# Kernel optimization log

Measured on AMD Instinct MI355X. Metric: run time of the kernel, lower is better.

Reference implementation:

```python
import jax, jax.numpy as jnp
import numpy as np
import math

D_MODEL = 1024
N_HEADS = 16
D_K = D_MODEL // N_HEADS
BS, SQ, SK = 2, 2048, 2048


def setup_inputs() -> dict:
    key = jax.random.key(0)
    ks = jax.random.split(key, 7)
    q = jax.random.normal(ks[0], (BS, SQ, D_MODEL), dtype=jnp.float32)
    k = jax.random.normal(ks[1], (BS, SK, D_MODEL), dtype=jnp.float32)
    v = jax.random.normal(ks[2], (BS, SK, D_MODEL), dtype=jnp.float32)
    # causal mask: True = masked out (matches torch masked_fill semantics)
    mask = jnp.broadcast_to(
        ~jnp.tril(jnp.ones((SQ, SK), dtype=bool)), (BS, SQ, SK))
    scale = 1.0 / math.sqrt(D_MODEL)
    wq = jax.random.normal(ks[3], (D_MODEL, D_MODEL), dtype=jnp.float32) * scale
    wk = jax.random.normal(ks[4], (D_MODEL, D_MODEL), dtype=jnp.float32) * scale
    wv = jax.random.normal(ks[5], (D_MODEL, D_MODEL), dtype=jnp.float32) * scale
    wo = jax.random.normal(ks[6], (D_MODEL, D_MODEL), dtype=jnp.float32) * scale
    return {"q": q, "k": k, "v": v, "mask": mask,
            "wq": wq, "wk": wk, "wv": wv, "wo": wo}


def reference(q, k, v, mask, wq, wk, wv, wo):
    bs, sq, _ = q.shape
    sk = k.shape[1]
    # nn.Linear(bias=False): x @ W.T ; reshape to heads -> [b, h, s, d_k]
    qh = (q @ wq.T).reshape(bs, sq, N_HEADS, D_K).transpose(0, 2, 1, 3)
    kh = (k @ wk.T).reshape(bs, sk, N_HEADS, D_K).transpose(0, 2, 1, 3)
    vh = (v @ wv.T).reshape(bs, sk, N_HEADS, D_K).transpose(0, 2, 1, 3)
    # scaled dot-product attention, full [b,h,sq,sk] scores (as original)
    z = jnp.einsum('bhqd,bhkd->bhqk', qh, kh) / math.sqrt(D_K)
    z = jnp.where(mask[:, None, :, :], jnp.float32(-1e10), z)
    z = jax.nn.softmax(z, axis=-1)
    z = jnp.einsum('bhqk,bhkd->bhqd', z, vh)
    z = z.transpose(0, 2, 1, 3).reshape(bs, sq, D_MODEL)
    return z @ wo.T
```

## Files before the change

### kernel.cpp

```cpp
#include <hip/hip_runtime.h>
#include <hip/hip_bf16.h>
#include <stdint.h>

typedef short s16x8 __attribute__((ext_vector_type(8)));
typedef float f32x4 __attribute__((ext_vector_type(4)));

#define BSZ 2
#define SQL 2048
#define DMODEL 1024
#define NHEAD 16
#define DKH 64

#if __has_builtin(__builtin_amdgcn_exp2f)
#define EXP2(x) __builtin_amdgcn_exp2f(x)
#else
#define EXP2(x) exp2f(x)
#endif

__device__ __forceinline__ ushort f2bf(float f) {
  uint32_t u = __float_as_uint(f);
  u += 0x7fffu + ((u >> 16) & 1u);
  return (ushort)(u >> 16);
}

__device__ __forceinline__ uint32_t cvtpk_bf16(float lo, float hi) {
  uint32_t r;
  asm("v_cvt_pk_bf16_f32 %0, %1, %2" : "=v"(r) : "v"(lo), "v"(hi));
  return r;
}

__device__ __forceinline__ float rowmax16(float x) {
  x = fmaxf(x, __int_as_float(__builtin_amdgcn_update_dpp(0, __float_as_int(x), 0x121, 0xf, 0xf, true)));
  x = fmaxf(x, __int_as_float(__builtin_amdgcn_update_dpp(0, __float_as_int(x), 0x122, 0xf, 0xf, true)));
  x = fmaxf(x, __int_as_float(__builtin_amdgcn_update_dpp(0, __float_as_int(x), 0x124, 0xf, 0xf, true)));
  x = fmaxf(x, __int_as_float(__builtin_amdgcn_update_dpp(0, __float_as_int(x), 0x128, 0xf, 0xf, true)));
  return x;
}

__device__ __forceinline__ void gload_lds16(const ushort* g, ushort* l) {
  __builtin_amdgcn_global_load_lds((const __attribute__((address_space(1))) void*)g,
                                   (__attribute__((address_space(3))) void*)l,
                                   16, 0, 0);
}

__global__ void cvt_all(const float* __restrict__ q, const float* __restrict__ k,
                        const float* __restrict__ v, const float* __restrict__ wq,
                        const float* __restrict__ wk, const float* __restrict__ wv,
                        const float* __restrict__ wo, ushort* __restrict__ dq,
                        ushort* __restrict__ dk, ushort* __restrict__ dv,
                        ushort* __restrict__ dwq, ushort* __restrict__ dwk,
                        ushort* __restrict__ dwv, ushort* __restrict__ dwo) {
  int b = blockIdx.x;
  const float* s; ushort* d; int off;
  if (b < 4096)       { s = q;  d = dq;  off = b; }
  else if (b < 8192)  { s = k;  d = dk;  off = b - 4096; }
  else if (b < 12288) { s = v;  d = dv;  off = b - 8192; }
  else if (b < 13312) { s = wq; d = dwq; off = b - 12288; }
  else if (b < 14336) { s = wk; d = dwk; off = b - 13312; }
  else if (b < 15360) { s = wv; d = dwv; off = b - 14336; }
  else                { s = wo; d = dwo; off = b - 15360; }
  int i = (off * 256 + threadIdx.x) * 4;
  float4 x = *(const float4*)(s + i);
  ushort4 o;
  o.x = f2bf(x.x); o.y = f2bf(x.y); o.z = f2bf(x.z); o.w = f2bf(x.w);
  *(ushort4*)(d + i) = o;
}

__device__ __forceinline__ void gemm_core(const ushort* __restrict__ A,
                                          const ushort* __restrict__ B,
                                          ushort* sA, ushort* sB, f32x4 (&acc)[4][4]) {
  const int t = threadIdx.x, w = t >> 6, lane = t & 63;
  const int lrow = lane & 15, lk = (lane >> 4) * 8;
  const int m0 = blockIdx.x * 128, n0 = blockIdx.y * 128;
  const int wm = (w >> 1) * 64, wn = (w & 1) * 64;

  auto stage = [&](int kt, int buf) {
#pragma unroll
    for (int i = 0; i < 2; ++i) {
      int ci = i * 256 + t;
      int row = ci >> 2;
      int ce = (ci & 3) * 8;
      gload_lds16(A + (size_t)(m0 + row) * 1024 + kt * 32 + ce,
                  sA + buf * 4096 + (i * 256 + w * 64) * 8);
      gload_lds16(B + (size_t)(n0 + row) * 1024 + kt * 32 + ce,
                  sB + buf * 4096 + (i * 256 + w * 64) * 8);
    }
  };

  stage(0, 0);
  for (int kt = 0; kt < 32; ++kt) {
    const int cur = kt & 1;
    if (kt < 31) {
      stage(kt + 1, cur ^ 1);
      asm volatile("s_waitcnt vmcnt(4)" ::: "memory");
    } else {
      asm volatile("s_waitcnt vmcnt(0)" ::: "memory");
    }
    __builtin_amdgcn_s_barrier();
    __builtin_amdgcn_sched_barrier(0);
    const ushort* pA = sA + cur * 4096;
    const ushort* pB = sB + cur * 4096;
    s16x8 af[4], bfr[4];
#pragma unroll
    for (int mi = 0; mi < 4; ++mi)
      af[mi] = *(const s16x8*)(pA + (wm + mi * 16 + lrow) * 32 + lk);
#pragma unroll
    for (int ni = 0; ni < 4; ++ni)
      bfr[ni] = *(const s16x8*)(pB + (wn + ni * 16 + lrow) * 32 + lk);
    __builtin_amdgcn_s_setprio(1);
#pragma unroll
    for (int mi = 0; mi < 4; ++mi)
#pragma unroll
      for (int ni = 0; ni < 4; ++ni)
        acc[mi][ni] = __builtin_amdgcn_mfma_f32_16x16x32_bf16(af[mi], bfr[ni], acc[mi][ni], 0, 0, 0);
    __builtin_amdgcn_s_setprio(0);
    asm volatile("s_waitcnt lgkmcnt(0)" ::: "memory");
    __builtin_amdgcn_s_barrier();
  }
}

__device__ __forceinline__ void epi_heads(f32x4 (&acc)[4][4], ushort* D, float scale, bool vtrans) {
  const int lane = threadIdx.x & 63, w = threadIdx.x >> 6;
  const int m0 = blockIdx.x * 128, n0 = blockIdx.y * 128;
  const int wm = (w >> 1) * 64, wn = (w & 1) * 64;
#pragma unroll
  for (int mi = 0; mi < 4; ++mi)
#pragma unroll
    for (int ni = 0; ni < 4; ++ni)
#pragma unroll
      for (int r = 0; r < 4; ++r) {
        int m = m0 + wm + mi * 16 + (lane >> 4) * 4 + r;
        int n = n0 + wn + ni * 16 + (lane & 15);
        ushort bv = f2bf(acc[mi][ni][r] * scale);
        int b = m >> 11, s = m & 2047, h = n >> 6, d = n & 63;
        if (vtrans)
          D[((size_t)((b * 16 + h) * 64 + d)) * 2048 + s] = bv;
        else
          D[((size_t)((b * 16 + h) * 2048 + s)) * 64 + d] = bv;
      }
}

__global__ __launch_bounds__(256) void gemm_qkv(const ushort* __restrict__ qb,
                                                const ushort* __restrict__ kb,
                                                const ushort* __restrict__ vb,
                                                const ushort* __restrict__ wqb,
                                                const ushort* __restrict__ wkb,
                                                const ushort* __restrict__ wvb,
                                                ushort* __restrict__ Qh,
                                                ushort* __restrict__ Kh,
                                                ushort* __restrict__ Vt) {
  __shared__ __align__(16) ushort sA[2 * 128 * 32];
  __shared__ __align__(16) ushort sB[2 * 128 * 32];
  const int z = blockIdx.z;
  const ushort* A = (z == 0) ? qb : (z == 1) ? kb : vb;
  const ushort* B = (z == 0) ? wqb : (z == 1) ? wkb : wvb;
  f32x4 acc[4][4] = {};
  gemm_core(A, B, sA, sB, acc);
  ushort* D = (z == 0) ? Qh : (z == 1) ? Kh : Vt;
  epi_heads(acc, D, (z == 0) ? 0.18033688f : 1.0f, z == 2);
}

__global__ __launch_bounds__(256) void gemm_out(const ushort* __restrict__ A,
                                                const ushort* __restrict__ B,
                                                float* __restrict__ D) {
  __shared__ __align__(16) ushort sA[2 * 128 * 32];
  __shared__ __align__(16) ushort sB[2 * 128 * 32];
  f32x4 acc[4][4] = {};
  gemm_core(A, B, sA, sB, acc);
  const int lane = threadIdx.x & 63, w = threadIdx.x >> 6;
  const int m0 = blockIdx.x * 128, n0 = blockIdx.y * 128;
  const int wm = (w >> 1) * 64, wn = (w & 1) * 64;
#pragma unroll
  for (int mi = 0; mi < 4; ++mi)
#pragma unroll
    for (int ni = 0; ni < 4; ++ni)
#pragma unroll
      for (int r = 0; r < 4; ++r) {
        int m = m0 + wm + mi * 16 + (lane >> 4) * 4 + r;
        int n = n0 + wn + ni * 16 + (lane & 15);
        D[(size_t)m * 1024 + n] = acc[mi][ni][r];
      }
}

__global__ __launch_bounds__(512) void attn_fwd(const ushort* __restrict__ Qh,
                                                const ushort* __restrict__ Kh,
                                                const ushort* __restrict__ Vt,
                                                ushort* __restrict__ Z) {
  __shared__ __align__(16) ushort sK[2][64 * 64];
  __shared__ __align__(16) ushort sV[2][64 * 64];
  __shared__ __align__(16) ushort sP[8][16 * 72];
  const int t = threadIdx.x, w = t >> 6, lane = t & 63;
  const int lcol = lane & 15, lhi = lane >> 4;
  const int p = blockIdx.x, bh = blockIdx.y;
  const int qlo = p, qhi = 31 - p;
  const int setid = w >> 2;
  const int qtile = setid ? qhi : qlo;
  const int qr0 = qtile * 64 + (w & 3) * 16;
  const ushort* Qb = Qh + (size_t)bh * SQL * DKH;
  const ushort* Kb = Kh + (size_t)bh * SQL * DKH;
  const ushort* Vb = Vt + (size_t)bh * DKH * SQL;

  s16x8 qf0, qf1;
  {
    const ushort* qp = Qb + (size_t)(qr0 + lcol) * DKH + lhi * 8;
    qf0 = *(const s16x8*)qp;
    qf1 = *(const s16x8*)(qp + 32);
  }
  float mr[4], lrp[4];
  f32x4 o[4] = {};
#pragma unroll
  for (int r = 0; r < 4; ++r) { mr[r] = -1e30f; lrp[r] = 0.f; }
  ushort* Pw = &sP[w][0];

  auto stage = [&](int kb, int buf) {
    int row = t >> 3, cc = t & 7;
    int scz = cc ^ (row & 7);
    gload_lds16(Kb + (size_t)(kb * 64 + row) * DKH + scz * 8, &sK[buf][w * 512]);
    gload_lds16(Vb + (size_t)row * SQL + kb * 64 + scz * 8, &sV[buf][w * 512]);
  };

  const int nkb = qhi + 1;
  stage(0, 0);
  for (int kb = 0; kb < nkb; ++kb) {
    const int cur = kb & 1;
    if (kb + 1 < nkb) {
      stage(kb + 1, cur ^ 1);
      asm volatile("s_waitcnt vmcnt(2)" ::: "memory");
    } else {
      asm volatile("s_waitcnt vmcnt(0)" ::: "memory");
    }
    __builtin_amdgcn_s_barrier();
    __builtin_amdgcn_sched_barrier(0);
    const bool act = setid || (kb <= qlo);
    if (act) {
      const ushort* pK = &sK[cur][0];
      const ushort* pV = &sV[cur][0];
      f32x4 sc4[4];
      __builtin_amdgcn_s_setprio(1);
#pragma unroll
      for (int ktt = 0; ktt < 4; ++ktt) {
        int row = ktt * 16 + lcol;
        int c0 = lhi ^ (row & 7);
        int c1 = (lhi + 4) ^ (row & 7);
        s16x8 k0 = *(const s16x8*)(pK + row * 64 + c0 * 8);
        s16x8 k1 = *(const s16x8*)(pK + row * 64 + c1 * 8);
        f32x4 a = {};
        a = __builtin_amdgcn_mfma_f32_16x16x32_bf16(qf0, k0, a, 0, 0, 0);
        a = __builtin_amdgcn_mfma_f32_16x16x32_bf16(qf1, k1, a, 0, 0, 0);
        sc4[ktt] = a;
      }
      __builtin_amdgcn_s_setprio(0);
      if (kb == qtile) {
#pragma unroll
        for (int ktt = 0; ktt < 4; ++ktt) {
          int kloc = ktt * 16 + lcol;
#pragma unroll
          for (int r = 0; r < 4; ++r)
            if (kloc > (w & 3) * 16 + lhi * 4 + r) sc4[ktt][r] = -1e30f;
        }
      }
      float tm4[4];
#pragma unroll
      for (int r = 0; r < 4; ++r) {
        float tm = fmaxf(fmaxf(sc4[0][r], sc4[1][r]), fmaxf(sc4[2][r], sc4[3][r]));
        tm4[r] = rowmax16(tm);
      }
      bool grow = (tm4[0] > mr[0] + 8.f) || (tm4[1] > mr[1] + 8.f) ||
                  (tm4[2] > mr[2] + 8.f) || (tm4[3] > mr[3] + 8.f);
      if (__any((int)grow)) {
#pragma unroll
        for (int r = 0; r < 4; ++r) {
          float mn = fmaxf(mr[r], tm4[r]);
          float al = EXP2(mr[r] - mn);
          lrp[r] *= al;
          o[0][r] *= al; o[1][r] *= al; o[2][r] *= al; o[3][r] *= al;
          mr[r] = mn;
        }
      }
#pragma unroll
      for (int r = 0; r < 4; ++r) {
        float p0 = EXP2(sc4[0][r] - mr[r]);
        float p1 = EXP2(sc4[1][r] - mr[r]);
        float p2 = EXP2(sc4[2][r] - mr[r]);
        float p3 = EXP2(sc4[3][r] - mr[r]);
        lrp[r] += (p0 + p1) + (p2 + p3);
        uint32_t w01 = cvtpk_bf16(p0, p1);
        uint32_t w23 = cvtpk_bf16(p2, p3);
        ushort* pr = Pw + (lhi * 4 + r) * 72 + lcol;
        pr[0]  = (ushort)(w01 & 0xffffu);
        pr[16] = (ushort)(w01 >> 16);
        pr[32] = (ushort)(w23 & 0xffffu);
        pr[48] = (ushort)(w23 >> 16);
      }
      __builtin_amdgcn_s_setprio(1);
#pragma unroll
      for (int kc = 0; kc < 2; ++kc) {
        s16x8 pf = *(const s16x8*)(Pw + lcol * 72 + kc * 32 + lhi * 8);
#pragma unroll
        for (int dt = 0; dt < 4; ++dt) {
          int row = dt * 16 + lcol;
          int cc = (lhi + 4 * kc) ^ (row & 7);
          s16x8 vf = *(const s16x8*)(pV + row * 64 + cc * 8);
          o[dt] = __builtin_amdgcn_mfma_f32_16x16x32_bf16(pf, vf, o[dt], 0, 0, 0);
        }
      }
      __builtin_amdgcn_s_setprio(0);
    }
    asm volatile("s_waitcnt lgkmcnt(0)" ::: "memory");
    __builtin_amdgcn_s_barrier();
  }

  const int b = bh >> 4, h = bh & 15;
#pragma unroll
  for (int r = 0; r < 4; ++r) {
    float sum = lrp[r];
    sum += __shfl_xor(sum, 1);
    sum += __shfl_xor(sum, 2);
    sum += __shfl_xor(sum, 4);
    sum += __shfl_xor(sum, 8);
    float inv = 1.0f / sum;
    int q = qr0 + lhi * 4 + r;
    size_t base = ((size_t)(b * SQL + q)) * DMODEL + h * DKH + lcol;
#pragma unroll
    for (int dt = 0; dt < 4; ++dt)
      Z[base + dt * 16] = f2bf(o[dt][r] * inv);
  }
}

extern "C" void kernel_launch(void* const* d_in, const int* in_sizes, int n_in,
                              void* d_out, int out_size, void* d_ws, size_t ws_size,
                              hipStream_t stream) {
  const float* q = (const float*)d_in[0];
  const float* k = (const float*)d_in[1];
  const float* v = (const float*)d_in[2];
  const float* wq = (const float*)d_in[4];
  const float* wk = (const float*)d_in[5];
  const float* wv = (const float*)d_in[6];
  const float* wo = (const float*)d_in[7];

  const size_t NBIG = (size_t)BSZ * SQL * DMODEL;
  const size_t NW = (size_t)DMODEL * DMODEL;
  ushort* qb = (ushort*)d_ws;
  ushort* kb = qb + NBIG;
  ushort* vb = kb + NBIG;
  ushort* wqb = vb + NBIG;
  ushort* wkb = wqb + NW;
  ushort* wvb = wkb + NW;
  ushort* wob = wvb + NW;
  ushort* Qh = wob + NW;
  ushort* Kh = Qh + NBIG;
  ushort* Vt = Kh + NBIG;
  ushort* Z  = Vt + NBIG;

  cvt_all<<<dim3(16384), 256, 0, stream>>>(q, k, v, wq, wk, wv, wo,
                                           qb, kb, vb, wqb, wkb, wvb, wob);
  gemm_qkv<<<dim3(32, 8, 3), 256, 0, stream>>>(qb, kb, vb, wqb, wkb, wvb, Qh, Kh, Vt);
  attn_fwd<<<dim3(16, BSZ * NHEAD), 512, 0, stream>>>(Qh, Kh, Vt, Z);
  gemm_out<<<dim3(32, 8), 256, 0, stream>>>(Z, wob, (float*)d_out);
}
```

Measured before the change: 132.0 us.

## Give each attention wave two query subtiles and shrink output GEMM tile

```diff
diff --git a/kernel.cpp b/kernel.cpp
--- a/kernel.cpp
+++ b/kernel.cpp
@@ -133,10 +133,12 @@
         int n = n0 + wn + ni * 16 + (lane & 15);
         ushort bv = f2bf(acc[mi][ni][r] * scale);
         int b = m >> 11, s = m & 2047, h = n >> 6, d = n & 63;
-        if (vtrans)
-          D[((size_t)((b * 16 + h) * 64 + d)) * 2048 + s] = bv;
-        else
+        if (vtrans) {
+          int sp = (s & ~63) | (((s & 15) << 2) | ((s >> 4) & 3));
+          D[((size_t)((b * 16 + h) * 64 + d)) * 2048 + sp] = bv;
+        } else {
           D[((size_t)((b * 16 + h) * 2048 + s)) * 64 + d] = bv;
+        }
       }
 }
 
@@ -160,18 +162,65 @@
   epi_heads(acc, D, (z == 0) ? 0.18033688f : 1.0f, z == 2);
 }
 
-__global__ __launch_bounds__(256) void gemm_out(const ushort* __restrict__ A,
-                                                const ushort* __restrict__ B,
-                                                float* __restrict__ D) {
-  __shared__ __align__(16) ushort sA[2 * 128 * 32];
+__global__ __launch_bounds__(256) void gemm_out64(const ushort* __restrict__ A,
+                                                  const ushort* __restrict__ B,
+                                                  float* __restrict__ D) {
+  __shared__ __align__(16) ushort sA[2 * 64 * 32];
   __shared__ __align__(16) ushort sB[2 * 128 * 32];
-  f32x4 acc[4][4] = {};
-  gemm_core(A, B, sA, sB, acc);
-  const int lane = threadIdx.x & 63, w = threadIdx.x >> 6;
-  const int m0 = blockIdx.x * 128, n0 = blockIdx.y * 128;
-  const int wm = (w >> 1) * 64, wn = (w & 1) * 64;
-#pragma unroll
-  for (int mi = 0; mi < 4; ++mi)
+  const int t = threadIdx.x, w = t >> 6, lane = t & 63;
+  const int lrow = lane & 15, lk = (lane >> 4) * 8;
+  const int m0 = blockIdx.x * 64, n0 = blockIdx.y * 128;
+  const int wm = (w >> 1) * 32, wn = (w & 1) * 64;
+  f32x4 acc[2][4] = {};
+
+  auto stage = [&](int kt, int buf) {
+    {
+      int row = t >> 2, ce = (t & 3) * 8;
+      gload_lds16(A + (size_t)(m0 + row) * 1024 + kt * 32 + ce,
+                  sA + buf * 2048 + (w * 64) * 8);
+    }
+#pragma unroll
+    for (int i = 0; i < 2; ++i) {
+      int ci = i * 256 + t;
+      int row = ci >> 2, ce = (ci & 3) * 8;
+      gload_lds16(B + (size_t)(n0 + row) * 1024 + kt * 32 + ce,
+                  sB + buf * 4096 + (i * 256 + w * 64) * 8);
+    }
+  };
+
+  stage(0, 0);
+  for (int kt = 0; kt < 32; ++kt) {
+    const int cur = kt & 1;
+    if (kt < 31) {
+      stage(kt + 1, cur ^ 1);
+      asm volatile("s_waitcnt vmcnt(3)" ::: "memory");
+    } else {
+      asm volatile("s_waitcnt vmcnt(0)" ::: "memory");
+    }
+    __builtin_amdgcn_s_barrier();
+    __builtin_amdgcn_sched_barrier(0);
+    const ushort* pA = sA + cur * 2048;
+    const ushort* pB = sB + cur * 4096;
+    s16x8 af[2], bfr[4];
+#pragma unroll
+    for (int mi = 0; mi < 2; ++mi)
+      af[mi] = *(const s16x8*)(pA + (wm + mi * 16 + lrow) * 32 + lk);
+#pragma unroll
+    for (int ni = 0; ni < 4; ++ni)
+      bfr[ni] = *(const s16x8*)(pB + (wn + ni * 16 + lrow) * 32 + lk);
+    __builtin_amdgcn_s_setprio(1);
+#pragma unroll
+    for (int mi = 0; mi < 2; ++mi)
+#pragma unroll
+      for (int ni = 0; ni < 4; ++ni)
+        acc[mi][ni] = __builtin_amdgcn_mfma_f32_16x16x32_bf16(af[mi], bfr[ni], acc[mi][ni], 0, 0, 0);
+    __builtin_amdgcn_s_setprio(0);
+    asm volatile("s_waitcnt lgkmcnt(0)" ::: "memory");
+    __builtin_amdgcn_s_barrier();
+  }
+
+#pragma unroll
+  for (int mi = 0; mi < 2; ++mi)
 #pragma unroll
     for (int ni = 0; ni < 4; ++ni)
 #pragma unroll
@@ -182,41 +231,48 @@
       }
 }
 
-__global__ __launch_bounds__(512) void attn_fwd(const ushort* __restrict__ Qh,
+__global__ __launch_bounds__(256) void attn_fwd(const ushort* __restrict__ Qh,
                                                 const ushort* __restrict__ Kh,
                                                 const ushort* __restrict__ Vt,
                                                 ushort* __restrict__ Z) {
   __shared__ __align__(16) ushort sK[2][64 * 64];
   __shared__ __align__(16) ushort sV[2][64 * 64];
-  __shared__ __align__(16) ushort sP[8][16 * 72];
+  __shared__ __align__(16) ushort sP[4][32 * 72];
   const int t = threadIdx.x, w = t >> 6, lane = t & 63;
   const int lcol = lane & 15, lhi = lane >> 4;
   const int p = blockIdx.x, bh = blockIdx.y;
   const int qlo = p, qhi = 31 - p;
-  const int setid = w >> 2;
+  const int setid = w >> 1;
   const int qtile = setid ? qhi : qlo;
-  const int qr0 = qtile * 64 + (w & 3) * 16;
+  const int qr0 = qtile * 64 + (w & 1) * 32;
   const ushort* Qb = Qh + (size_t)bh * SQL * DKH;
   const ushort* Kb = Kh + (size_t)bh * SQL * DKH;
   const ushort* Vb = Vt + (size_t)bh * DKH * SQL;
 
-  s16x8 qf0, qf1;
-  {
-    const ushort* qp = Qb + (size_t)(qr0 + lcol) * DKH + lhi * 8;
-    qf0 = *(const s16x8*)qp;
-    qf1 = *(const s16x8*)(qp + 32);
+  s16x8 qf[2][2];
+#pragma unroll
+  for (int s = 0; s < 2; ++s) {
+    const ushort* qp = Qb + (size_t)(qr0 + s * 16 + lcol) * DKH + lhi * 8;
+    qf[s][0] = *(const s16x8*)qp;
+    qf[s][1] = *(const s16x8*)(qp + 32);
   }
-  float mr[4], lrp[4];
-  f32x4 o[4] = {};
-#pragma unroll
-  for (int r = 0; r < 4; ++r) { mr[r] = -1e30f; lrp[r] = 0.f; }
+  float mr[2][4], lrp[2][4];
+  f32x4 o[2][4] = {};
+#pragma unroll
+  for (int s = 0; s < 2; ++s)
+#pragma unroll
+    for (int r = 0; r < 4; ++r) { mr[s][r] = -1e30f; lrp[s][r] = 0.f; }
   ushort* Pw = &sP[w][0];
 
   auto stage = [&](int kb, int buf) {
-    int row = t >> 3, cc = t & 7;
-    int scz = cc ^ (row & 7);
-    gload_lds16(Kb + (size_t)(kb * 64 + row) * DKH + scz * 8, &sK[buf][w * 512]);
-    gload_lds16(Vb + (size_t)row * SQL + kb * 64 + scz * 8, &sV[buf][w * 512]);
+#pragma unroll
+    for (int i = 0; i < 2; ++i) {
+      int ci = i * 256 + t;
+      int row = ci >> 3, cc = ci & 7;
+      int scz = cc ^ (row & 7);
+      gload_lds16(Kb + (size_t)(kb * 64 + row) * DKH + scz * 8, &sK[buf][(i * 256 + w * 64) * 8]);
+      gload_lds16(Vb + (size_t)row * SQL + kb * 64 + scz * 8, &sV[buf][(i * 256 + w * 64) * 8]);
+    }
   };
 
   const int nkb = qhi + 1;
@@ -225,7 +281,7 @@
     const int cur = kb & 1;
     if (kb + 1 < nkb) {
       stage(kb + 1, cur ^ 1);
-      asm volatile("s_waitcnt vmcnt(2)" ::: "memory");
+      asm volatile("s_waitcnt vmcnt(4)" ::: "memory");
     } else {
       asm volatile("s_waitcnt vmcnt(0)" ::: "memory");
     }
@@ -235,7 +291,7 @@
     if (act) {
       const ushort* pK = &sK[cur][0];
       const ushort* pV = &sV[cur][0];
-      f32x4 sc4[4];
+      f32x4 scs[2][4];
       __builtin_amdgcn_s_setprio(1);
 #pragma unroll
       for (int ktt = 0; ktt < 4; ++ktt) {
@@ -245,63 +301,72 @@
         s16x8 k0 = *(const s16x8*)(pK + row * 64 + c0 * 8);
         s16x8 k1 = *(const s16x8*)(pK + row * 64 + c1 * 8);
         f32x4 a = {};
-        a = __builtin_amdgcn_mfma_f32_16x16x32_bf16(qf0, k0, a, 0, 0, 0);
-        a = __builtin_amdgcn_mfma_f32_16x16x32_bf16(qf1, k1, a, 0, 0, 0);
-        sc4[ktt] = a;
+        a = __builtin_amdgcn_mfma_f32_16x16x32_bf16(qf[0][0], k0, a, 0, 0, 0);
+        a = __builtin_amdgcn_mfma_f32_16x16x32_bf16(qf[0][1], k1, a, 0, 0, 0);
+        scs[0][ktt] = a;
+        f32x4 b2 = {};
+        b2 = __builtin_amdgcn_mfma_f32_16x16x32_bf16(qf[1][0], k0, b2, 0, 0, 0);
+        b2 = __builtin_amdgcn_mfma_f32_16x16x32_bf16(qf[1][1], k1, b2, 0, 0, 0);
+        scs[1][ktt] = b2;
       }
       __builtin_amdgcn_s_setprio(0);
       if (kb == qtile) {
 #pragma unroll
-        for (int ktt = 0; ktt < 4; ++ktt) {
-          int kloc = ktt * 16 + lcol;
-#pragma unroll
-          for (int r = 0; r < 4; ++r)
-            if (kloc > (w & 3) * 16 + lhi * 4 + r) sc4[ktt][r] = -1e30f;
+        for (int s = 0; s < 2; ++s)
+#pragma unroll
+          for (int ktt = 0; ktt < 4; ++ktt) {
+            int kloc = ktt * 16 + lcol;
+#pragma unroll
+            for (int r = 0; r < 4; ++r)
+              if (kloc > (w & 1) * 32 + s * 16 + lhi * 4 + r) scs[s][ktt][r] = -1e30f;
+          }
+      }
+#pragma unroll
+      for (int s = 0; s < 2; ++s) {
+        float tm4[4];
+#pragma unroll
+        for (int r = 0; r < 4; ++r) {
+          float tm = fmaxf(fmaxf(scs[s][0][r], scs[s][1][r]), fmaxf(scs[s][2][r], scs[s][3][r]));
+          tm4[r] = rowmax16(tm);
         }
-      }
-      float tm4[4];
-#pragma unroll
-      for (int r = 0; r < 4; ++r) {
-        float tm = fmaxf(fmaxf(sc4[0][r], sc4[1][r]), fmaxf(sc4[2][r], sc4[3][r]));
-        tm4[r] = rowmax16(tm);
-      }
-      bool grow = (tm4[0] > mr[0] + 8.f) || (tm4[1] > mr[1] + 8.f) ||
-                  (tm4[2] > mr[2] + 8.f) || (tm4[3] > mr[3] + 8.f);
-      if (__any((int)grow)) {
+        bool grow = (tm4[0] > mr[s][0] + 8.f) || (tm4[1] > mr[s][1] + 8.f) ||
+                    (tm4[2] > mr[s][2] + 8.f) || (tm4[3] > mr[s][3] + 8.f);
+        if (__any((int)grow)) {
+#pragma unroll
+          for (int r = 0; r < 4; ++r) {
+            float mn = fmaxf(mr[s][r], tm4[r]);
+            float al = EXP2(mr[s][r] - mn);
+            lrp[s][r] *= al;
+            o[s][0][r] *= al; o[s][1][r] *= al; o[s][2][r] *= al; o[s][3][r] *= al;
+            mr[s][r] = mn;
+          }
+        }
+        ushort* Pws = Pw + s * 16 * 72;
 #pragma unroll
         for (int r = 0; r < 4; ++r) {
-          float mn = fmaxf(mr[r], tm4[r]);
-          float al = EXP2(mr[r] - mn);
-          lrp[r] *= al;
-          o[0][r] *= al; o[1][r] *= al; o[2][r] *= al; o[3][r] *= al;
-          mr[r] = mn;
+          float p0 = EXP2(scs[s][0][r] - mr[s][r]);
+          float p1 = EXP2(scs[s][1][r] - mr[s][r]);
+          float p2 = EXP2(scs[s][2][r] - mr[s][r]);
+          float p3 = EXP2(scs[s][3][r] - mr[s][r]);
+          lrp[s][r] += (p0 + p1) + (p2 + p3);
+          uint2 pk;
+          pk.x = cvtpk_bf16(p0, p1);
+          pk.y = cvtpk_bf16(p2, p3);
+          *(uint2*)(Pws + (lhi * 4 + r) * 72 + lcol * 4) = pk;
         }
       }
-#pragma unroll
-      for (int r = 0; r < 4; ++r) {
-        float p0 = EXP2(sc4[0][r] - mr[r]);
-        float p1 = EXP2(sc4[1][r] - mr[r]);
-        float p2 = EXP2(sc4[2][r] - mr[r]);
-        float p3 = EXP2(sc4[3][r] - mr[r]);
-        lrp[r] += (p0 + p1) + (p2 + p3);
-        uint32_t w01 = cvtpk_bf16(p0, p1);
-        uint32_t w23 = cvtpk_bf16(p2, p3);
-        ushort* pr = Pw + (lhi * 4 + r) * 72 + lcol;
-        pr[0]  = (ushort)(w01 & 0xffffu);
-        pr[16] = (ushort)(w01 >> 16);
-        pr[32] = (ushort)(w23 & 0xffffu);
-        pr[48] = (ushort)(w23 >> 16);
-      }
       __builtin_amdgcn_s_setprio(1);
 #pragma unroll
       for (int kc = 0; kc < 2; ++kc) {
-        s16x8 pf = *(const s16x8*)(Pw + lcol * 72 + kc * 32 + lhi * 8);
+        s16x8 pfA = *(const s16x8*)(Pw + lcol * 72 + kc * 32 + lhi * 8);
+        s16x8 pfB = *(const s16x8*)(Pw + (16 + lcol) * 72 + kc * 32 + lhi * 8);
 #pragma unroll
         for (int dt = 0; dt < 4; ++dt) {
           int row = dt * 16 + lcol;
           int cc = (lhi + 4 * kc) ^ (row & 7);
           s16x8 vf = *(const s16x8*)(pV + row * 64 + cc * 8);
-          o[dt] = __builtin_amdgcn_mfma_f32_16x16x32_bf16(pf, vf, o[dt], 0, 0, 0);
+          o[0][dt] = __builtin_amdgcn_mfma_f32_16x16x32_bf16(pfA, vf, o[0][dt], 0, 0, 0);
+          o[1][dt] = __builtin_amdgcn_mfma_f32_16x16x32_bf16(pfB, vf, o[1][dt], 0, 0, 0);
         }
       }
       __builtin_amdgcn_s_setprio(0);
@@ -312,18 +377,21 @@
 
   const int b = bh >> 4, h = bh & 15;
 #pragma unroll
-  for (int r = 0; r < 4; ++r) {
-    float sum = lrp[r];
-    sum += __shfl_xor(sum, 1);
-    sum += __shfl_xor(sum, 2);
-    sum += __shfl_xor(sum, 4);
-    sum += __shfl_xor(sum, 8);
-    float inv = 1.0f / sum;
-    int q = qr0 + lhi * 4 + r;
-    size_t base = ((size_t)(b * SQL + q)) * DMODEL + h * DKH + lcol;
-#pragma unroll
-    for (int dt = 0; dt < 4; ++dt)
-      Z[base + dt * 16] = f2bf(o[dt][r] * inv);
+  for (int s = 0; s < 2; ++s) {
+#pragma unroll
+    for (int r = 0; r < 4; ++r) {
+      float sum = lrp[s][r];
+      sum += __shfl_xor(sum, 1);
+      sum += __shfl_xor(sum, 2);
+      sum += __shfl_xor(sum, 4);
+      sum += __shfl_xor(sum, 8);
+      float inv = 1.0f / sum;
+      int q = qr0 + s * 16 + lhi * 4 + r;
+      size_t base = ((size_t)(b * SQL + q)) * DMODEL + h * DKH + lcol;
+#pragma unroll
+      for (int dt = 0; dt < 4; ++dt)
+        Z[base + dt * 16] = f2bf(o[s][dt][r] * inv);
+    }
   }
 }
 
@@ -355,6 +423,6 @@
   cvt_all<<<dim3(16384), 256, 0, stream>>>(q, k, v, wq, wk, wv, wo,
                                            qb, kb, vb, wqb, wkb, wvb, wob);
   gemm_qkv<<<dim3(32, 8, 3), 256, 0, stream>>>(qb, kb, vb, wqb, wkb, wvb, Qh, Kh, Vt);
-  attn_fwd<<<dim3(16, BSZ * NHEAD), 512, 0, stream>>>(Qh, Kh, Vt, Z);
-  gemm_out<<<dim3(32, 8), 256, 0, stream>>>(Z, wob, (float*)d_out);
-}
+  attn_fwd<<<dim3(16, BSZ * NHEAD), 256, 0, stream>>>(Qh, Kh, Vt, Z);
+  gemm_out64<<<dim3(64, 8), 256, 0, stream>>>(Z, wob, (float*)d_out);
+}
```

After: 153.8 us. 16.5% more time.

## Fuse activation fp32-to-bf16 conversion into QKV GEMM and shrink output GEMM tiles

Applied to the files above, without the earlier changes.

```diff
diff --git a/kernel.cpp b/kernel.cpp
--- a/kernel.cpp
+++ b/kernel.cpp
@@ -43,80 +43,17 @@
                                    16, 0, 0);
 }
 
-__global__ void cvt_all(const float* __restrict__ q, const float* __restrict__ k,
-                        const float* __restrict__ v, const float* __restrict__ wq,
-                        const float* __restrict__ wk, const float* __restrict__ wv,
-                        const float* __restrict__ wo, ushort* __restrict__ dq,
-                        ushort* __restrict__ dk, ushort* __restrict__ dv,
-                        ushort* __restrict__ dwq, ushort* __restrict__ dwk,
-                        ushort* __restrict__ dwv, ushort* __restrict__ dwo) {
-  int b = blockIdx.x;
-  const float* s; ushort* d; int off;
-  if (b < 4096)       { s = q;  d = dq;  off = b; }
-  else if (b < 8192)  { s = k;  d = dk;  off = b - 4096; }
-  else if (b < 12288) { s = v;  d = dv;  off = b - 8192; }
-  else if (b < 13312) { s = wq; d = dwq; off = b - 12288; }
-  else if (b < 14336) { s = wk; d = dwk; off = b - 13312; }
-  else if (b < 15360) { s = wv; d = dwv; off = b - 14336; }
-  else                { s = wo; d = dwo; off = b - 15360; }
-  int i = (off * 256 + threadIdx.x) * 4;
+__global__ void cvt_w(const float* __restrict__ wq, const float* __restrict__ wk,
+                      const float* __restrict__ wv, const float* __restrict__ wo,
+                      ushort* __restrict__ dwq, ushort* __restrict__ dwk,
+                      ushort* __restrict__ dwv, ushort* __restrict__ dwo) {
+  const float* s = (blockIdx.y == 0) ? wq : (blockIdx.y == 1) ? wk : (blockIdx.y == 2) ? wv : wo;
+  ushort* d = (blockIdx.y == 0) ? dwq : (blockIdx.y == 1) ? dwk : (blockIdx.y == 2) ? dwv : dwo;
+  int i = (blockIdx.x * 256 + threadIdx.x) * 4;
   float4 x = *(const float4*)(s + i);
   ushort4 o;
   o.x = f2bf(x.x); o.y = f2bf(x.y); o.z = f2bf(x.z); o.w = f2bf(x.w);
   *(ushort4*)(d + i) = o;
-}
-
-__device__ __forceinline__ void gemm_core(const ushort* __restrict__ A,
-                                          const ushort* __restrict__ B,
-                                          ushort* sA, ushort* sB, f32x4 (&acc)[4][4]) {
-  const int t = threadIdx.x, w = t >> 6, lane = t & 63;
-  const int lrow = lane & 15, lk = (lane >> 4) * 8;
-  const int m0 = blockIdx.x * 128, n0 = blockIdx.y * 128;
-  const int wm = (w >> 1) * 64, wn = (w & 1) * 64;
-
-  auto stage = [&](int kt, int buf) {
-#pragma unroll
-    for (int i = 0; i < 2; ++i) {
-      int ci = i * 256 + t;
-      int row = ci >> 2;
-      int ce = (ci & 3) * 8;
-      gload_lds16(A + (size_t)(m0 + row) * 1024 + kt * 32 + ce,
-                  sA + buf * 4096 + (i * 256 + w * 64) * 8);
-      gload_lds16(B + (size_t)(n0 + row) * 1024 + kt * 32 + ce,
-                  sB + buf * 4096 + (i * 256 + w * 64) * 8);
-    }
-  };
-
-  stage(0, 0);
-  for (int kt = 0; kt < 32; ++kt) {
-    const int cur = kt & 1;
-    if (kt < 31) {
-      stage(kt + 1, cur ^ 1);
-      asm volatile("s_waitcnt vmcnt(4)" ::: "memory");
-    } else {
-      asm volatile("s_waitcnt vmcnt(0)" ::: "memory");
-    }
-    __builtin_amdgcn_s_barrier();
-    __builtin_amdgcn_sched_barrier(0);
-    const ushort* pA = sA + cur * 4096;
-    const ushort* pB = sB + cur * 4096;
-    s16x8 af[4], bfr[4];
-#pragma unroll
-    for (int mi = 0; mi < 4; ++mi)
-      af[mi] = *(const s16x8*)(pA + (wm + mi * 16 + lrow) * 32 + lk);
-#pragma unroll
-    for (int ni = 0; ni < 4; ++ni)
-      bfr[ni] = *(const s16x8*)(pB + (wn + ni * 16 + lrow) * 32 + lk);
-    __builtin_amdgcn_s_setprio(1);
-#pragma unroll
-    for (int mi = 0; mi < 4; ++mi)
-#pragma unroll
-      for (int ni = 0; ni < 4; ++ni)
-        acc[mi][ni] = __builtin_amdgcn_mfma_f32_16x16x32_bf16(af[mi], bfr[ni], acc[mi][ni], 0, 0, 0);
-    __builtin_amdgcn_s_setprio(0);
-    asm volatile("s_waitcnt lgkmcnt(0)" ::: "memory");
-    __builtin_amdgcn_s_barrier();
-  }
 }
 
 __device__ __forceinline__ void epi_heads(f32x4 (&acc)[4][4], ushort* D, float scale, bool vtrans) {
@@ -133,45 +70,166 @@
         int n = n0 + wn + ni * 16 + (lane & 15);
         ushort bv = f2bf(acc[mi][ni][r] * scale);
         int b = m >> 11, s = m & 2047, h = n >> 6, d = n & 63;
-        if (vtrans)
-          D[((size_t)((b * 16 + h) * 64 + d)) * 2048 + s] = bv;
-        else
+        if (vtrans) {
+          int sp = (s & ~63) | (((s & 15) << 2) | ((s >> 4) & 3));
+          D[((size_t)((b * 16 + h) * 64 + d)) * 2048 + sp] = bv;
+        } else {
           D[((size_t)((b * 16 + h) * 2048 + s)) * 64 + d] = bv;
-      }
-}
-
-__global__ __launch_bounds__(256) void gemm_qkv(const ushort* __restrict__ qb,
-                                                const ushort* __restrict__ kb,
-                                                const ushort* __restrict__ vb,
+        }
+      }
+}
+
+__global__ __launch_bounds__(256) void gemm_qkv(const float* __restrict__ qf,
+                                                const float* __restrict__ kf,
+                                                const float* __restrict__ vf,
                                                 const ushort* __restrict__ wqb,
                                                 const ushort* __restrict__ wkb,
                                                 const ushort* __restrict__ wvb,
                                                 ushort* __restrict__ Qh,
                                                 ushort* __restrict__ Kh,
                                                 ushort* __restrict__ Vt) {
-  __shared__ __align__(16) ushort sA[2 * 128 * 32];
-  __shared__ __align__(16) ushort sB[2 * 128 * 32];
+  __shared__ __align__(16) ushort sA[2 * 4096];
+  __shared__ __align__(16) ushort sB[2 * 4096];
   const int z = blockIdx.z;
-  const ushort* A = (z == 0) ? qb : (z == 1) ? kb : vb;
+  const float* A = (z == 0) ? qf : (z == 1) ? kf : vf;
   const ushort* B = (z == 0) ? wqb : (z == 1) ? wkb : wvb;
+  const int t = threadIdx.x, w = t >> 6, lane = t & 63;
+  const int lrow = lane & 15, lk = (lane >> 4) * 8;
+  const int m0 = blockIdx.x * 128, n0 = blockIdx.y * 128;
+  const int wm = (w >> 1) * 64, wn = (w & 1) * 64;
   f32x4 acc[4][4] = {};
-  gemm_core(A, B, sA, sB, acc);
+
+  const int rowa = t >> 2, cea = (t & 3) * 8;
+  const float* A0 = A + (size_t)(m0 + rowa) * 1024 + cea;
+  const float* A1 = A0 + (size_t)64 * 1024;
+  const int la0 = t * 8, la1 = (256 + t) * 8;
+
+  float4 a00, a01, a10, a11;
+  auto issueA = [&](int kt) {
+    a00 = *(const float4*)(A0 + kt * 32);
+    a01 = *(const float4*)(A0 + kt * 32 + 4);
+    a10 = *(const float4*)(A1 + kt * 32);
+    a11 = *(const float4*)(A1 + kt * 32 + 4);
+  };
+  auto writeA = [&](int buf) {
+    uint4 u0, u1;
+    u0.x = cvtpk_bf16(a00.x, a00.y); u0.y = cvtpk_bf16(a00.z, a00.w);
+    u0.z = cvtpk_bf16(a01.x, a01.y); u0.w = cvtpk_bf16(a01.z, a01.w);
+    u1.x = cvtpk_bf16(a10.x, a10.y); u1.y = cvtpk_bf16(a10.z, a10.w);
+    u1.z = cvtpk_bf16(a11.x, a11.y); u1.w = cvtpk_bf16(a11.z, a11.w);
+    *(uint4*)(sA + buf * 4096 + la0) = u0;
+    *(uint4*)(sA + buf * 4096 + la1) = u1;
+  };
+  auto gloadB = [&](int kt, int buf) {
+#pragma unroll
+    for (int i = 0; i < 2; ++i) {
+      int ci = i * 256 + t, row = ci >> 2, ce = (ci & 3) * 8;
+      gload_lds16(B + (size_t)(n0 + row) * 1024 + kt * 32 + ce,
+                  sB + buf * 4096 + (i * 256 + w * 64) * 8);
+    }
+  };
+
+  issueA(0);
+  gloadB(0, 0);
+  writeA(0);
+  asm volatile("s_waitcnt lgkmcnt(0)" ::: "memory");
+
+  for (int kt = 0; kt < 32; ++kt) {
+    const int cur = kt & 1;
+    if (kt < 31) {
+      issueA(kt + 1);
+      __builtin_amdgcn_sched_barrier(0);
+      gloadB(kt + 1, cur ^ 1);
+      asm volatile("s_waitcnt vmcnt(6)" ::: "memory");
+    } else {
+      asm volatile("s_waitcnt vmcnt(0)" ::: "memory");
+    }
+    __builtin_amdgcn_s_barrier();
+    __builtin_amdgcn_sched_barrier(0);
+    const ushort* pA = sA + cur * 4096;
+    const ushort* pB = sB + cur * 4096;
+    s16x8 af[4], bfr[4];
+#pragma unroll
+    for (int mi = 0; mi < 4; ++mi)
+      af[mi] = *(const s16x8*)(pA + (wm + mi * 16 + lrow) * 32 + lk);
+#pragma unroll
+    for (int ni = 0; ni < 4; ++ni)
+      bfr[ni] = *(const s16x8*)(pB + (wn + ni * 16 + lrow) * 32 + lk);
+    __builtin_amdgcn_s_setprio(1);
+#pragma unroll
+    for (int mi = 0; mi < 4; ++mi)
+#pragma unroll
+      for (int ni = 0; ni < 4; ++ni)
+        acc[mi][ni] = __builtin_amdgcn_mfma_f32_16x16x32_bf16(af[mi], bfr[ni], acc[mi][ni], 0, 0, 0);
+    __builtin_amdgcn_s_setprio(0);
+    if (kt < 31) writeA(cur ^ 1);
+    asm volatile("s_waitcnt lgkmcnt(0)" ::: "memory");
+    __builtin_amdgcn_s_barrier();
+  }
+
   ushort* D = (z == 0) ? Qh : (z == 1) ? Kh : Vt;
   epi_heads(acc, D, (z == 0) ? 0.18033688f : 1.0f, z == 2);
 }
 
-__global__ __launch_bounds__(256) void gemm_out(const ushort* __restrict__ A,
-                                                const ushort* __restrict__ B,
-                                                float* __restrict__ D) {
-  __shared__ __align__(16) ushort sA[2 * 128 * 32];
+__global__ __launch_bounds__(256) void gemm_out64(const ushort* __restrict__ A,
+                                                  const ushort* __restrict__ B,
+                                                  float* __restrict__ D) {
+  __shared__ __align__(16) ushort sA[2 * 64 * 32];
   __shared__ __align__(16) ushort sB[2 * 128 * 32];
-  f32x4 acc[4][4] = {};
-  gemm_core(A, B, sA, sB, acc);
-  const int lane = threadIdx.x & 63, w = threadIdx.x >> 6;
-  const int m0 = blockIdx.x * 128, n0 = blockIdx.y * 128;
-  const int wm = (w >> 1) * 64, wn = (w & 1) * 64;
-#pragma unroll
-  for (int mi = 0; mi < 4; ++mi)
+  const int t = threadIdx.x, w = t >> 6, lane = t & 63;
+  const int lrow = lane & 15, lk = (lane >> 4) * 8;
+  const int m0 = blockIdx.x * 64, n0 = blockIdx.y * 128;
+  const int wm = (w >> 1) * 32, wn = (w & 1) * 64;
+  f32x4 acc[2][4] = {};
+
+  auto stage = [&](int kt, int buf) {
+    {
+      int row = t >> 2, ce = (t & 3) * 8;
+      gload_lds16(A + (size_t)(m0 + row) * 1024 + kt * 32 + ce,
+                  sA + buf * 2048 + (w * 64) * 8);
+    }
+#pragma unroll
+    for (int i = 0; i < 2; ++i) {
+      int ci = i * 256 + t;
+      int row = ci >> 2, ce = (ci & 3) * 8;
+      gload_lds16(B + (size_t)(n0 + row) * 1024 + kt * 32 + ce,
+                  sB + buf * 4096 + (i * 256 + w * 64) * 8);
+    }
+  };
+
+  stage(0, 0);
+  for (int kt = 0; kt < 32; ++kt) {
+    const int cur = kt & 1;
+    if (kt < 31) {
+      stage(kt + 1, cur ^ 1);
+      asm volatile("s_waitcnt vmcnt(3)" ::: "memory");
+    } else {
+      asm volatile("s_waitcnt vmcnt(0)" ::: "memory");
+    }
+    __builtin_amdgcn_s_barrier();
+    __builtin_amdgcn_sched_barrier(0);
+    const ushort* pA = sA + cur * 2048;
+    const ushort* pB = sB + cur * 4096;
+    s16x8 af[2], bfr[4];
+#pragma unroll
+    for (int mi = 0; mi < 2; ++mi)
+      af[mi] = *(const s16x8*)(pA + (wm + mi * 16 + lrow) * 32 + lk);
+#pragma unroll
+    for (int ni = 0; ni < 4; ++ni)
+      bfr[ni] = *(const s16x8*)(pB + (wn + ni * 16 + lrow) * 32 + lk);
+    __builtin_amdgcn_s_setprio(1);
+#pragma unroll
+    for (int mi = 0; mi < 2; ++mi)
+#pragma unroll
+      for (int ni = 0; ni < 4; ++ni)
+        acc[mi][ni] = __builtin_amdgcn_mfma_f32_16x16x32_bf16(af[mi], bfr[ni], acc[mi][ni], 0, 0, 0);
+    __builtin_amdgcn_s_setprio(0);
+    asm volatile("s_waitcnt lgkmcnt(0)" ::: "memory");
+    __builtin_amdgcn_s_barrier();
+  }
+
+#pragma unroll
+  for (int mi = 0; mi < 2; ++mi)
 #pragma unroll
     for (int ni = 0; ni < 4; ++ni)
 #pragma unroll
@@ -284,13 +342,10 @@
         float p2 = EXP2(sc4[2][r] - mr[r]);
         float p3 = EXP2(sc4[3][r] - mr[r]);
         lrp[r] += (p0 + p1) + (p2 + p3);
-        uint32_t w01 = cvtpk_bf16(p0, p1);
-        uint32_t w23 = cvtpk_bf16(p2, p3);
-        ushort* pr = Pw + (lhi * 4 + r) * 72 + lcol;
-        pr[0]  = (ushort)(w01 & 0xffffu);
-        pr[16] = (ushort)(w01 >> 16);
-        pr[32] = (ushort)(w23 & 0xffffu);
-        pr[48] = (ushort)(w23 >> 16);
+        uint2 pk;
+        pk.x = cvtpk_bf16(p0, p1);
+        pk.y = cvtpk_bf16(p2, p3);
+        *(uint2*)(Pw + (lhi * 4 + r) * 72 + lcol * 4) = pk;
       }
       __builtin_amdgcn_s_setprio(1);
 #pragma unroll
@@ -340,10 +395,7 @@
 
   const size_t NBIG = (size_t)BSZ * SQL * DMODEL;
   const size_t NW = (size_t)DMODEL * DMODEL;
-  ushort* qb = (ushort*)d_ws;
-  ushort* kb = qb + NBIG;
-  ushort* vb = kb + NBIG;
-  ushort* wqb = vb + NBIG;
+  ushort* wqb = (ushort*)d_ws;
   ushort* wkb = wqb + NW;
   ushort* wvb = wkb + NW;
   ushort* wob = wvb + NW;
@@ -352,9 +404,8 @@
   ushort* Vt = Kh + NBIG;
   ushort* Z  = Vt + NBIG;
 
-  cvt_all<<<dim3(16384), 256, 0, stream>>>(q, k, v, wq, wk, wv, wo,
-                                           qb, kb, vb, wqb, wkb, wvb, wob);
-  gemm_qkv<<<dim3(32, 8, 3), 256, 0, stream>>>(qb, kb, vb, wqb, wkb, wvb, Qh, Kh, Vt);
+  cvt_w<<<dim3(1024, 4), 256, 0, stream>>>(wq, wk, wv, wo, wqb, wkb, wvb, wob);
+  gemm_qkv<<<dim3(32, 8, 3), 256, 0, stream>>>(q, k, v, wqb, wkb, wvb, Qh, Kh, Vt);
   attn_fwd<<<dim3(16, BSZ * NHEAD), 512, 0, stream>>>(Qh, Kh, Vt, Z);
-  gemm_out<<<dim3(32, 8), 256, 0, stream>>>(Z, wob, (float*)d_out);
-}
+  gemm_out64<<<dim3(64, 8), 256, 0, stream>>>(Z, wob, (float*)d_out);
+}
```

New measurement: 125.5 us. 4.9% less time.
